# Kernel optimization log

Hardware: AMD Instinct MI355X
Metric: run time of the kernel (lower is better)

The kernel has to match this reference:

```python
import jax, jax.numpy as jnp
import numpy as np


def setup_inputs() -> dict:
    key = jax.random.key(0)
    ks = jax.random.split(key, 8)
    B, L, D = 64, 1024, 1280
    rep = jax.random.normal(ks[0], (B, L, D), dtype=jnp.float32)
    # token counts include BOS/EOS; span 1:len-1 must be non-empty -> len >= 3
    batch_len = jax.random.randint(ks[1], (B,), 3, L + 1, dtype=jnp.int32)
    s = 0.02
    W1 = jax.random.normal(ks[2], (1280, 640), dtype=jnp.float32) * s
    b1 = jnp.zeros((640,), dtype=jnp.float32)
    W2 = jax.random.normal(ks[3], (640, 320), dtype=jnp.float32) * s
    b2 = jnp.zeros((320,), dtype=jnp.float32)
    W3 = jax.random.normal(ks[4], (320, 2), dtype=jnp.float32) * s
    b3 = jnp.zeros((2,), dtype=jnp.float32)
    return {"rep": rep, "batch_len": batch_len, "W1": W1, "b1": b1,
            "W2": W2, "b2": b2, "W3": W3, "b3": b3}


def _ragged_mean(rep, batch_len):
    # mean over positions 1 .. len-2 (skip BOS token and final EOS token)
    B, L, D = rep.shape
    pos = jnp.arange(L)[None, :]                      # [1, L]
    lo = jnp.int32(1)
    hi = (batch_len - 1)[:, None]                     # exclusive upper bound
    mask = (pos >= lo) & (pos < hi)                   # [B, L]
    maskf = mask.astype(rep.dtype)
    summed = jnp.einsum('bld,bl->bd', rep, maskf)     # fused masked sum
    count = jnp.maximum(maskf.sum(axis=1, keepdims=True), 1.0)
    return summed / count                             # [B, D]


def reference(rep, batch_len, W1, b1, W2, b2, W3, b3):
    pooled = _ragged_mean(rep, batch_len)             # [B, 1280]
    # predictor MLP (dropout is identity in eval mode)
    h = jax.nn.relu(pooled @ W1 + b1)                 # [B, 640]
    emb = jax.nn.relu(h @ W2 + b2)                    # [B, 320]
    y = emb @ W3 + b3                                 # [B, 2]
    return (y, emb)
```

## Files before the change

### kernel.cpp

```cpp
#include <hip/hip_runtime.h>

#define B_     64
#define L_     1024
#define D_     1280
#define H1_    640
#define H2_    320
#define NSPLIT 32
#define KS_    16
#define KC_    80
#define NJT_   10
#define NJT2_  5

__global__ void pool_partial(const float* __restrict__ rep, const int* __restrict__ blen,
                             float* __restrict__ part) {
    const int s   = blockIdx.x;
    const int b   = blockIdx.y;
    const int tid = threadIdx.x;
    const int n   = blen[b] - 2;

    const int l0 = 1 + (s * n) / NSPLIT;
    const int l1 = 1 + ((s + 1) * n) / NSPLIT;

    float4 acc = make_float4(0.f, 0.f, 0.f, 0.f);
    const float4* base = (const float4*)rep + (size_t)b * L_ * (D_ / 4) + tid;
    #pragma unroll 8
    for (int l = l0; l < l1; ++l) {
        float4 v = base[(size_t)l * (D_ / 4)];
        acc.x += v.x; acc.y += v.y; acc.z += v.z; acc.w += v.w;
    }
    ((float4*)part)[((size_t)b * NSPLIT + s) * (D_ / 4) + tid] = acc;
}

__global__ void pool_reduce(const float* __restrict__ part, const int* __restrict__ blen,
                            float* __restrict__ pooled) {
    const int qt  = blockIdx.x;
    const int b   = blockIdx.y;
    const int tid = threadIdx.x;
    const int col = qt * 64 + tid;

    int n = blen[b] - 2; if (n < 1) n = 1;
    const float inv = 1.0f / (float)n;
    const float4* p = (const float4*)part + (size_t)b * NSPLIT * (D_ / 4) + col;
    float4 a = make_float4(0.f, 0.f, 0.f, 0.f);
    #pragma unroll
    for (int s = 0; s < NSPLIT; ++s) {
        float4 v = p[(size_t)s * (D_ / 4)];
        a.x += v.x; a.y += v.y; a.z += v.z; a.w += v.w;
    }
    ((float4*)pooled)[(size_t)b * (D_ / 4) + col] =
        make_float4(a.x * inv, a.y * inv, a.z * inv, a.w * inv);
}

__global__ void mlp1_partial(const float* __restrict__ pooled, const float* __restrict__ W1,
                             float* __restrict__ hpart) {
    const int jt  = blockIdx.x;
    const int ks  = blockIdx.y;
    const int tid = threadIdx.x;
    const int jl  = tid & 63;
    const int b0  = (tid >> 6) * 8;
    const int k0  = ks * KC_;
    const int j0  = jt * 64;

    __shared__ float pl[B_][KC_];
    for (int e = tid; e < B_ * (KC_ / 4); e += 512) {
        const int b   = e / (KC_ / 4);
        const int kk4 = e % (KC_ / 4);
        float4 v = ((const float4*)pooled)[(size_t)b * (D_ / 4) + (k0 / 4) + kk4];
        *(float4*)&pl[b][kk4 * 4] = v;
    }
    __syncthreads();

    float acc[8];
    #pragma unroll
    for (int r = 0; r < 8; ++r) acc[r] = 0.f;

    const float* w1p = W1 + (size_t)k0 * H1_ + j0 + jl;
    for (int kk = 0; kk < KC_; kk += 4) {
        const float w0 = w1p[(size_t)(kk + 0) * H1_];
        const float w1 = w1p[(size_t)(kk + 1) * H1_];
        const float w2 = w1p[(size_t)(kk + 2) * H1_];
        const float w3 = w1p[(size_t)(kk + 3) * H1_];
        #pragma unroll
        for (int r = 0; r < 8; ++r) {
            float4 pv = *(const float4*)&pl[b0 + r][kk];
            acc[r] = fmaf(pv.x, w0, acc[r]);
            acc[r] = fmaf(pv.y, w1, acc[r]);
            acc[r] = fmaf(pv.z, w2, acc[r]);
            acc[r] = fmaf(pv.w, w3, acc[r]);
        }
    }
    float* hp = hpart + (size_t)ks * B_ * H1_;
    #pragma unroll
    for (int r = 0; r < 8; ++r)
        hp[(size_t)(b0 + r) * H1_ + j0 + jl] = acc[r];
}

__global__ void mlp2(const float* __restrict__ hpart, const float* __restrict__ b1,
                     const float* __restrict__ W2, const float* __restrict__ b2,
                     float* __restrict__ out) {
    const int jt  = blockIdx.x;
    const int b   = blockIdx.y;
    const int tid = threadIdx.x;
    const int jl  = tid & 63;
    const int kq  = tid >> 6;
    const int j   = jt * 64 + jl;

    __shared__ float hrow[H1_];
    __shared__ float pt[8][64];

    for (int jj = tid; jj < H1_; jj += 512) {
        float s = b1[jj];
        #pragma unroll
        for (int ks = 0; ks < KS_; ++ks)
            s += hpart[((size_t)ks * B_ + b) * H1_ + jj];
        hrow[jj] = fmaxf(s, 0.f);
    }
    __syncthreads();

    float a0 = 0.f, a1 = 0.f, a2 = 0.f, a3 = 0.f;
    const int kbeg = kq * (H1_ / 8);
    const float* w = W2 + (size_t)kbeg * H2_ + j;
    #pragma unroll 5
    for (int k = 0; k < H1_ / 8; k += 4) {
        const float4 hv = *(const float4*)&hrow[kbeg + k];
        a0 = fmaf(hv.x, w[(size_t)(k + 0) * H2_], a0);
        a1 = fmaf(hv.y, w[(size_t)(k + 1) * H2_], a1);
        a2 = fmaf(hv.z, w[(size_t)(k + 2) * H2_], a2);
        a3 = fmaf(hv.w, w[(size_t)(k + 3) * H2_], a3);
    }
    pt[kq][jl] = (a0 + a1) + (a2 + a3);
    __syncthreads();

    if (tid < 64) {
        float e = b2[j];
        #pragma unroll
        for (int q = 0; q < 8; ++q) e += pt[q][jl];
        out[128 + (size_t)b * H2_ + j] = fmaxf(e, 0.f);
    }
}

__global__ void mlp3(const float* __restrict__ out_emb, const float* __restrict__ W3,
                     const float* __restrict__ b3, float* __restrict__ out) {
    const int b    = blockIdx.x;
    const int lane = threadIdx.x;
    float s0 = 0.f, s1 = 0.f;
    #pragma unroll
    for (int i = 0; i < H2_ / 64; ++i) {
        const int jj = lane + i * 64;
        const float e = out_emb[128 + (size_t)b * H2_ + jj];
        s0 = fmaf(e, W3[(size_t)jj * 2 + 0], s0);
        s1 = fmaf(e, W3[(size_t)jj * 2 + 1], s1);
    }
    #pragma unroll
    for (int off = 32; off >= 1; off >>= 1) {
        s0 += __shfl_xor(s0, off, 64);
        s1 += __shfl_xor(s1, off, 64);
    }
    if (lane == 0) {
        out[(size_t)b * 2 + 0] = s0 + b3[0];
        out[(size_t)b * 2 + 1] = s1 + b3[1];
    }
}

extern "C" void kernel_launch(void* const* d_in, const int* in_sizes, int n_in,
                              void* d_out, int out_size, void* d_ws, size_t ws_size,
                              hipStream_t stream) {
    const float* rep  = (const float*)d_in[0];
    const int*   blen = (const int*)  d_in[1];
    const float* W1   = (const float*)d_in[2];
    const float* b1   = (const float*)d_in[3];
    const float* W2   = (const float*)d_in[4];
    const float* b2   = (const float*)d_in[5];
    const float* W3   = (const float*)d_in[6];
    const float* b3   = (const float*)d_in[7];
    float* out = (float*)d_out;

    float* ws     = (float*)d_ws;
    float* part   = ws;
    float* pooled = part + (size_t)B_ * NSPLIT * D_;
    float* hpart  = pooled + (size_t)B_ * D_;

    pool_partial<<<dim3(NSPLIT, B_), 320, 0, stream>>>(rep, blen, part);
    pool_reduce <<<dim3(5, B_), 64, 0, stream>>>(part, blen, pooled);
    mlp1_partial<<<dim3(NJT_, KS_), 512, 0, stream>>>(pooled, W1, hpart);
    mlp2        <<<dim3(NJT2_, B_), 512, 0, stream>>>(hpart, b1, W2, b2, out);
    mlp3        <<<B_, 64, 0, stream>>>(out, W3, b3, out);
}
```

Baseline: 50.72 us.

## Fuse pooling reduce into MLP1 and fold MLP3 into MLP2 via last-block counter

The partial-sum reduction of the pooled mean now happens inside the first MLP layer kernel, one block per (k-chunk, batch). That kernel reduces its 80-column slice of the 32 partial sums and multiplies it against the matching W1 rows, so the pooled buffer and one launch are gone. The final 320x2 projection moves into the second MLP kernel: an atomic counter per batch row, reset in pool_partial, picks the last finishing block to compute y. Kernel launches drop from five to three. In exchange, W1 is now re-read once per batch row (64 times instead of the earlier batched reuse across rows), and a threadfence plus atomic is added to the second kernel.

```diff
diff --git a/kernel.cpp b/kernel.cpp
--- a/kernel.cpp
+++ b/kernel.cpp
@@ -8,16 +8,17 @@
 #define NSPLIT 32
 #define KS_    16
 #define KC_    80
-#define NJT_   10
 #define NJT2_  5
 
 __global__ void pool_partial(const float* __restrict__ rep, const int* __restrict__ blen,
-                             float* __restrict__ part) {
+                             float* __restrict__ part, unsigned int* __restrict__ ctr2) {
     const int s   = blockIdx.x;
     const int b   = blockIdx.y;
     const int tid = threadIdx.x;
-    const int n   = blen[b] - 2;
 
+    if (s == 0 && tid == 0) ctr2[b] = 0u;
+
+    const int n  = blen[b] - 2;
     const int l0 = 1 + (s * n) / NSPLIT;
     const int l1 = 1 + ((s + 1) * n) / NSPLIT;
 
@@ -31,73 +32,60 @@
     ((float4*)part)[((size_t)b * NSPLIT + s) * (D_ / 4) + tid] = acc;
 }
 
-__global__ void pool_reduce(const float* __restrict__ part, const int* __restrict__ blen,
-                            float* __restrict__ pooled) {
-    const int qt  = blockIdx.x;
+__global__ void reduce_mlp1(const float* __restrict__ part, const int* __restrict__ blen,
+                            const float* __restrict__ W1, float* __restrict__ hpart) {
+    const int ks  = blockIdx.x;
     const int b   = blockIdx.y;
     const int tid = threadIdx.x;
-    const int col = qt * 64 + tid;
+    const int k0  = ks * KC_;
 
-    int n = blen[b] - 2; if (n < 1) n = 1;
-    const float inv = 1.0f / (float)n;
-    const float4* p = (const float4*)part + (size_t)b * NSPLIT * (D_ / 4) + col;
-    float4 a = make_float4(0.f, 0.f, 0.f, 0.f);
-    #pragma unroll
-    for (int s = 0; s < NSPLIT; ++s) {
-        float4 v = p[(size_t)s * (D_ / 4)];
-        a.x += v.x; a.y += v.y; a.z += v.z; a.w += v.w;
+    __shared__ float ptl[4][KC_];
+    __shared__ float pl[KC_];
+
+    {
+        const int q = tid / KC_;
+        const int c = tid - q * KC_;
+        const float* p = part + ((size_t)b * NSPLIT + q * 8) * D_ + k0 + c;
+        float s = 0.f;
+        #pragma unroll
+        for (int ss = 0; ss < 8; ++ss)
+            s += p[(size_t)ss * D_];
+        ptl[q][c] = s;
     }
-    ((float4*)pooled)[(size_t)b * (D_ / 4) + col] =
-        make_float4(a.x * inv, a.y * inv, a.z * inv, a.w * inv);
-}
-
-__global__ void mlp1_partial(const float* __restrict__ pooled, const float* __restrict__ W1,
-                             float* __restrict__ hpart) {
-    const int jt  = blockIdx.x;
-    const int ks  = blockIdx.y;
-    const int tid = threadIdx.x;
-    const int jl  = tid & 63;
-    const int b0  = (tid >> 6) * 8;
-    const int k0  = ks * KC_;
-    const int j0  = jt * 64;
-
-    __shared__ float pl[B_][KC_];
-    for (int e = tid; e < B_ * (KC_ / 4); e += 512) {
-        const int b   = e / (KC_ / 4);
-        const int kk4 = e % (KC_ / 4);
-        float4 v = ((const float4*)pooled)[(size_t)b * (D_ / 4) + (k0 / 4) + kk4];
-        *(float4*)&pl[b][kk4 * 4] = v;
+    __syncthreads();
+    if (tid < KC_) {
+        int n = blen[b] - 2; if (n < 1) n = 1;
+        pl[tid] = (ptl[0][tid] + ptl[1][tid] + ptl[2][tid] + ptl[3][tid]) / (float)n;
     }
     __syncthreads();
 
-    float acc[8];
-    #pragma unroll
-    for (int r = 0; r < 8; ++r) acc[r] = 0.f;
+    const int jl = tid & 63;
+    const int g  = tid >> 6;
+    const int j1 = g * 128 + jl;
+    const int j2 = j1 + 64;
 
-    const float* w1p = W1 + (size_t)k0 * H1_ + j0 + jl;
+    float a1x = 0.f, a1y = 0.f, a2x = 0.f, a2y = 0.f;
     for (int kk = 0; kk < KC_; kk += 4) {
-        const float w0 = w1p[(size_t)(kk + 0) * H1_];
-        const float w1 = w1p[(size_t)(kk + 1) * H1_];
-        const float w2 = w1p[(size_t)(kk + 2) * H1_];
-        const float w3 = w1p[(size_t)(kk + 3) * H1_];
-        #pragma unroll
-        for (int r = 0; r < 8; ++r) {
-            float4 pv = *(const float4*)&pl[b0 + r][kk];
-            acc[r] = fmaf(pv.x, w0, acc[r]);
-            acc[r] = fmaf(pv.y, w1, acc[r]);
-            acc[r] = fmaf(pv.z, w2, acc[r]);
-            acc[r] = fmaf(pv.w, w3, acc[r]);
-        }
+        const float4 pv = *(const float4*)&pl[kk];
+        const float* w = W1 + (size_t)(k0 + kk) * H1_;
+        a1x = fmaf(pv.x, w[j1],            a1x);
+        a1y = fmaf(pv.y, w[H1_ + j1],      a1y);
+        a1x = fmaf(pv.z, w[2 * H1_ + j1],  a1x);
+        a1y = fmaf(pv.w, w[3 * H1_ + j1],  a1y);
+        a2x = fmaf(pv.x, w[j2],            a2x);
+        a2y = fmaf(pv.y, w[H1_ + j2],      a2y);
+        a2x = fmaf(pv.z, w[2 * H1_ + j2],  a2x);
+        a2y = fmaf(pv.w, w[3 * H1_ + j2],  a2y);
     }
-    float* hp = hpart + (size_t)ks * B_ * H1_;
-    #pragma unroll
-    for (int r = 0; r < 8; ++r)
-        hp[(size_t)(b0 + r) * H1_ + j0 + jl] = acc[r];
+    float* hp = hpart + ((size_t)ks * B_ + b) * H1_;
+    hp[j1] = a1x + a1y;
+    hp[j2] = a2x + a2y;
 }
 
-__global__ void mlp2(const float* __restrict__ hpart, const float* __restrict__ b1,
-                     const float* __restrict__ W2, const float* __restrict__ b2,
-                     float* __restrict__ out) {
+__global__ void mlp2y(const float* __restrict__ hpart, const float* __restrict__ b1,
+                      const float* __restrict__ W2, const float* __restrict__ b2,
+                      const float* __restrict__ W3, const float* __restrict__ b3,
+                      float* __restrict__ out, unsigned int* __restrict__ ctr2) {
     const int jt  = blockIdx.x;
     const int b   = blockIdx.y;
     const int tid = threadIdx.x;
@@ -137,28 +125,36 @@
         for (int q = 0; q < 8; ++q) e += pt[q][jl];
         out[128 + (size_t)b * H2_ + j] = fmaxf(e, 0.f);
     }
-}
 
-__global__ void mlp3(const float* __restrict__ out_emb, const float* __restrict__ W3,
-                     const float* __restrict__ b3, float* __restrict__ out) {
-    const int b    = blockIdx.x;
-    const int lane = threadIdx.x;
-    float s0 = 0.f, s1 = 0.f;
-    #pragma unroll
-    for (int i = 0; i < H2_ / 64; ++i) {
-        const int jj = lane + i * 64;
-        const float e = out_emb[128 + (size_t)b * H2_ + jj];
-        s0 = fmaf(e, W3[(size_t)jj * 2 + 0], s0);
-        s1 = fmaf(e, W3[(size_t)jj * 2 + 1], s1);
+    __threadfence();
+    __syncthreads();
+    __shared__ unsigned int lastf;
+    if (tid == 0) {
+        unsigned int old = atomicAdd(&ctr2[b], 1u);
+        lastf = (old == (unsigned)(NJT2_ - 1)) ? 1u : 0u;
     }
-    #pragma unroll
-    for (int off = 32; off >= 1; off >>= 1) {
-        s0 += __shfl_xor(s0, off, 64);
-        s1 += __shfl_xor(s1, off, 64);
-    }
-    if (lane == 0) {
-        out[(size_t)b * 2 + 0] = s0 + b3[0];
-        out[(size_t)b * 2 + 1] = s1 + b3[1];
+    __syncthreads();
+
+    if (lastf && tid < 64) {
+        __threadfence();
+        const int lane = tid;
+        float s0 = 0.f, s1 = 0.f;
+        #pragma unroll
+        for (int i = 0; i < H2_ / 64; ++i) {
+            const int jj = lane + i * 64;
+            const float e = out[128 + (size_t)b * H2_ + jj];
+            s0 = fmaf(e, W3[(size_t)jj * 2 + 0], s0);
+            s1 = fmaf(e, W3[(size_t)jj * 2 + 1], s1);
+        }
+        #pragma unroll
+        for (int off = 32; off >= 1; off >>= 1) {
+            s0 += __shfl_xor(s0, off, 64);
+            s1 += __shfl_xor(s1, off, 64);
+        }
+        if (lane == 0) {
+            out[(size_t)b * 2 + 0] = s0 + b3[0];
+            out[(size_t)b * 2 + 1] = s1 + b3[1];
+        }
     }
 }
 
@@ -175,14 +171,12 @@
     const float* b3   = (const float*)d_in[7];
     float* out = (float*)d_out;
 
-    float* ws     = (float*)d_ws;
-    float* part   = ws;
-    float* pooled = part + (size_t)B_ * NSPLIT * D_;
-    float* hpart  = pooled + (size_t)B_ * D_;
+    float*        ws    = (float*)d_ws;
+    float*        part  = ws;
+    float*        hpart = part + (size_t)B_ * NSPLIT * D_;
+    unsigned int* ctr2  = (unsigned int*)(hpart + (size_t)KS_ * B_ * H1_);
 
-    pool_partial<<<dim3(NSPLIT, B_), 320, 0, stream>>>(rep, blen, part);
-    pool_reduce <<<dim3(5, B_), 64, 0, stream>>>(part, blen, pooled);
-    mlp1_partial<<<dim3(NJT_, KS_), 512, 0, stream>>>(pooled, W1, hpart);
-    mlp2        <<<dim3(NJT2_, B_), 512, 0, stream>>>(hpart, b1, W2, b2, out);
-    mlp3        <<<B_, 64, 0, stream>>>(out, W3, b3, out);
+    pool_partial<<<dim3(NSPLIT, B_), 320, 0, stream>>>(rep, blen, part, ctr2);
+    reduce_mlp1 <<<dim3(KS_, B_), 320, 0, stream>>>(part, blen, W1, hpart);
+    mlp2y       <<<dim3(NJT2_, B_), 512, 0, stream>>>(hpart, b1, W2, b2, W3, b3, out, ctr2);
 }
```

New measurement: 88.17 us. +73.8%, slower.

## Fuse MLP split-K reductions into producer kernels via last-block atomic counters

Applied to the files above, without the earlier changes.

Merges the split-K reduction of the first MLP layer into mlp1 using a per-tile atomic counter, so the last arriving block sums the partials, adds the bias and writes the ReLU hidden row. It also folds the final 320x2 projection into mlp2 with a per-batch counter, removing the mlp3 launch. Counters are reset inside pool_partial so no extra memset launch is needed. The intent is to cut one kernel launch and the redundant per-block hpart reduction in mlp2, at the cost of threadfences and atomics plus serialized tail work in the last block.

```diff
diff --git a/kernel.cpp b/kernel.cpp
--- a/kernel.cpp
+++ b/kernel.cpp
@@ -12,12 +12,18 @@
 #define NJT2_  5
 
 __global__ void pool_partial(const float* __restrict__ rep, const int* __restrict__ blen,
-                             float* __restrict__ part) {
+                             float* __restrict__ part, unsigned int* __restrict__ ctr1,
+                             unsigned int* __restrict__ ctr2) {
     const int s   = blockIdx.x;
     const int b   = blockIdx.y;
     const int tid = threadIdx.x;
-    const int n   = blen[b] - 2;
-
+
+    if (s == 0 && tid == 0) {
+        ctr2[b] = 0u;
+        if (b < NJT_) ctr1[b] = 0u;
+    }
+
+    const int n  = blen[b] - 2;
     const int l0 = 1 + (s * n) / NSPLIT;
     const int l1 = 1 + ((s + 1) * n) / NSPLIT;
 
@@ -51,8 +57,9 @@
         make_float4(a.x * inv, a.y * inv, a.z * inv, a.w * inv);
 }
 
-__global__ void mlp1_partial(const float* __restrict__ pooled, const float* __restrict__ W1,
-                             float* __restrict__ hpart) {
+__global__ void mlp1h(const float* __restrict__ pooled, const float* __restrict__ W1,
+                      const float* __restrict__ b1, float* __restrict__ hpart,
+                      float* __restrict__ hrow, unsigned int* __restrict__ ctr1) {
     const int jt  = blockIdx.x;
     const int ks  = blockIdx.y;
     const int tid = threadIdx.x;
@@ -93,11 +100,35 @@
     #pragma unroll
     for (int r = 0; r < 8; ++r)
         hp[(size_t)(b0 + r) * H1_ + j0 + jl] = acc[r];
-}
-
-__global__ void mlp2(const float* __restrict__ hpart, const float* __restrict__ b1,
-                     const float* __restrict__ W2, const float* __restrict__ b2,
-                     float* __restrict__ out) {
+
+    __threadfence();
+    __syncthreads();
+    __shared__ unsigned int lastf;
+    if (tid == 0) {
+        unsigned int old = atomicAdd(&ctr1[jt], 1u);
+        lastf = (old == (unsigned)(KS_ - 1)) ? 1u : 0u;
+    }
+    __syncthreads();
+
+    if (lastf) {
+        __threadfence();
+        const float bias = b1[j0 + jl];
+        #pragma unroll
+        for (int r = 0; r < 8; ++r) {
+            const int b = b0 + r;
+            float s = bias;
+            #pragma unroll
+            for (int k2 = 0; k2 < KS_; ++k2)
+                s += hpart[((size_t)k2 * B_ + b) * H1_ + j0 + jl];
+            hrow[(size_t)b * H1_ + j0 + jl] = fmaxf(s, 0.f);
+        }
+    }
+}
+
+__global__ void mlp2y(const float* __restrict__ hrow, const float* __restrict__ W2,
+                      const float* __restrict__ b2, const float* __restrict__ W3,
+                      const float* __restrict__ b3, float* __restrict__ out,
+                      unsigned int* __restrict__ ctr2) {
     const int jt  = blockIdx.x;
     const int b   = blockIdx.y;
     const int tid = threadIdx.x;
@@ -105,16 +136,11 @@
     const int kq  = tid >> 6;
     const int j   = jt * 64 + jl;
 
-    __shared__ float hrow[H1_];
+    __shared__ float hr[H1_];
     __shared__ float pt[8][64];
 
-    for (int jj = tid; jj < H1_; jj += 512) {
-        float s = b1[jj];
-        #pragma unroll
-        for (int ks = 0; ks < KS_; ++ks)
-            s += hpart[((size_t)ks * B_ + b) * H1_ + jj];
-        hrow[jj] = fmaxf(s, 0.f);
-    }
+    for (int jj = tid; jj < H1_; jj += 512)
+        hr[jj] = hrow[(size_t)b * H1_ + jj];
     __syncthreads();
 
     float a0 = 0.f, a1 = 0.f, a2 = 0.f, a3 = 0.f;
@@ -122,7 +148,7 @@
     const float* w = W2 + (size_t)kbeg * H2_ + j;
     #pragma unroll 5
     for (int k = 0; k < H1_ / 8; k += 4) {
-        const float4 hv = *(const float4*)&hrow[kbeg + k];
+        const float4 hv = *(const float4*)&hr[kbeg + k];
         a0 = fmaf(hv.x, w[(size_t)(k + 0) * H2_], a0);
         a1 = fmaf(hv.y, w[(size_t)(k + 1) * H2_], a1);
         a2 = fmaf(hv.z, w[(size_t)(k + 2) * H2_], a2);
@@ -137,28 +163,36 @@
         for (int q = 0; q < 8; ++q) e += pt[q][jl];
         out[128 + (size_t)b * H2_ + j] = fmaxf(e, 0.f);
     }
-}
-
-__global__ void mlp3(const float* __restrict__ out_emb, const float* __restrict__ W3,
-                     const float* __restrict__ b3, float* __restrict__ out) {
-    const int b    = blockIdx.x;
-    const int lane = threadIdx.x;
-    float s0 = 0.f, s1 = 0.f;
-    #pragma unroll
-    for (int i = 0; i < H2_ / 64; ++i) {
-        const int jj = lane + i * 64;
-        const float e = out_emb[128 + (size_t)b * H2_ + jj];
-        s0 = fmaf(e, W3[(size_t)jj * 2 + 0], s0);
-        s1 = fmaf(e, W3[(size_t)jj * 2 + 1], s1);
-    }
-    #pragma unroll
-    for (int off = 32; off >= 1; off >>= 1) {
-        s0 += __shfl_xor(s0, off, 64);
-        s1 += __shfl_xor(s1, off, 64);
-    }
-    if (lane == 0) {
-        out[(size_t)b * 2 + 0] = s0 + b3[0];
-        out[(size_t)b * 2 + 1] = s1 + b3[1];
+
+    __threadfence();
+    __syncthreads();
+    __shared__ unsigned int lastf;
+    if (tid == 0) {
+        unsigned int old = atomicAdd(&ctr2[b], 1u);
+        lastf = (old == (unsigned)(NJT2_ - 1)) ? 1u : 0u;
+    }
+    __syncthreads();
+
+    if (lastf && tid < 64) {
+        __threadfence();
+        const int lane = tid;
+        float s0 = 0.f, s1 = 0.f;
+        #pragma unroll
+        for (int i = 0; i < H2_ / 64; ++i) {
+            const int jj = lane + i * 64;
+            const float e = out[128 + (size_t)b * H2_ + jj];
+            s0 = fmaf(e, W3[(size_t)jj * 2 + 0], s0);
+            s1 = fmaf(e, W3[(size_t)jj * 2 + 1], s1);
+        }
+        #pragma unroll
+        for (int off = 32; off >= 1; off >>= 1) {
+            s0 += __shfl_xor(s0, off, 64);
+            s1 += __shfl_xor(s1, off, 64);
+        }
+        if (lane == 0) {
+            out[(size_t)b * 2 + 0] = s0 + b3[0];
+            out[(size_t)b * 2 + 1] = s1 + b3[1];
+        }
     }
 }
 
@@ -175,14 +209,16 @@
     const float* b3   = (const float*)d_in[7];
     float* out = (float*)d_out;
 
-    float* ws     = (float*)d_ws;
-    float* part   = ws;
-    float* pooled = part + (size_t)B_ * NSPLIT * D_;
-    float* hpart  = pooled + (size_t)B_ * D_;
-
-    pool_partial<<<dim3(NSPLIT, B_), 320, 0, stream>>>(rep, blen, part);
+    float*        ws     = (float*)d_ws;
+    float*        part   = ws;
+    float*        pooled = part + (size_t)B_ * NSPLIT * D_;
+    float*        hpart  = pooled + (size_t)B_ * D_;
+    float*        hrow   = hpart + (size_t)KS_ * B_ * H1_;
+    unsigned int* ctr1   = (unsigned int*)(hrow + (size_t)B_ * H1_);
+    unsigned int* ctr2   = ctr1 + NJT_;
+
+    pool_partial<<<dim3(NSPLIT, B_), 320, 0, stream>>>(rep, blen, part, ctr1, ctr2);
     pool_reduce <<<dim3(5, B_), 64, 0, stream>>>(part, blen, pooled);
-    mlp1_partial<<<dim3(NJT_, KS_), 512, 0, stream>>>(pooled, W1, hpart);
-    mlp2        <<<dim3(NJT2_, B_), 512, 0, stream>>>(hpart, b1, W2, b2, out);
-    mlp3        <<<B_, 64, 0, stream>>>(out, W3, b3, out);
-}
+    mlp1h       <<<dim3(NJT_, KS_), 512, 0, stream>>>(pooled, W1, b1, hpart, hrow, ctr1);
+    mlp2y       <<<dim3(NJT2_, B_), 512, 0, stream>>>(hrow, W2, b2, W3, b3, out, ctr2);
+}
```

Result: slower. 119.5 us (+135.6%).
